# Optimization experiments

Measured on AMD Instinct MI355X. Metric: run time of the kernel, lower is better.

## Reference

```python
import jax, jax.numpy as jnp
import numpy as np

B, N, EN, EE = 2, 512, 128, 64
F = 64          # out_features * num_heads (shared by node and edge projections)
H = 8           # num_heads
D_NODE = 8.0    # out_node_features (softmax scale)
D_EDGE = 8.0    # out_edge_features (softmax scale)


def setup_inputs() -> dict:
    key = jax.random.key(0)
    ks = jax.random.split(key, 6)
    nodes = jax.random.normal(ks[0], (B, N, EN), dtype=jnp.float32)
    edges = jax.random.normal(ks[1], (B, N, N, EE), dtype=jnp.float32)
    node_mask = jnp.ones((B, N), dtype=bool)
    node_W = jax.random.normal(ks[2], (EN, F), dtype=jnp.float32) / np.sqrt(EN)
    node_b = jnp.zeros((F,), dtype=jnp.float32)
    edge_W = jax.random.normal(ks[3], (EE, F), dtype=jnp.float32) / np.sqrt(EE)
    edge_b = jnp.zeros((F,), dtype=jnp.float32)
    att_W = jax.random.normal(ks[4], (F, H), dtype=jnp.float32) / np.sqrt(F)
    return {"nodes": nodes, "edges": edges, "node_mask": node_mask,
            "node_W": node_W, "node_b": node_b,
            "edge_W": edge_W, "edge_b": edge_b, "att_W": att_W}


def reference(nodes, edges, node_mask, node_W, node_b, edge_W, edge_b, att_W):
    nf = nodes @ node_W + node_b                      # [b,n,F]
    ef = edges @ edge_W + edge_b                      # [b,n,n,F]
    q = nf @ att_W                                    # [b,n,H]
    eq = ef @ att_W                                   # [b,n,n,H]
    sn = jnp.einsum('bik,bjk->bij', q, q) / jnp.sqrt(jnp.float32(D_NODE))
    se = jnp.einsum('bik,bijk->bij', q, eq) / jnp.sqrt(jnp.float32(D_EDGE))
    m = node_mask[..., None].astype(sn.dtype)         # [b,n,1] (mask multiplies scores, as in source)
    wn = jax.nn.softmax(sn * m, axis=-1)              # [b,n,n]
    we = jax.nn.softmax(se * m, axis=-1)              # [b,n,n]
    awn = jnp.einsum('bij,bik->bjk', wn, nf)          # [b,n,F]
    aef = jnp.einsum('bij,bijk->bik', we, ef)         # [b,n,F]
    updated_nodes = nf + awn + aef
    awe = we[..., None] * ef                          # [b,n,n,F]
    anf = jnp.einsum('bij,bik->bijk', wn, nf)         # [b,n,n,F]
    updated_edges = ef + awe + anf
    out_nodes = jax.nn.elu(updated_nodes)
    out_edges = jax.nn.elu(updated_edges).reshape(edges.shape[0], edges.shape[1], edges.shape[2], -1)
    return out_nodes, out_edges
```

## Files before the change

kernel.cpp:

```cpp
#include <hip/hip_runtime.h>
#include <stdint.h>

#define BB 2
#define NN 512
#define ENF 128
#define EEF 64
#define FF 64
#define HH 8

#define WS_NF    0
#define WS_Q     65536
#define WS_V     73728
#define WS_EW    139264
#define WS_EB    143360
#define WS_M     143424
#define WS_STATS 143936
#define WS_FLAG  145984
#define WS_EWFH  145992
#define WS_EWFL  150088
#define WS_TOTAL 154184

__device__ __align__(16) float g_ws[WS_TOTAL];

using short8  = __attribute__((ext_vector_type(8))) short;
using floatx4 = __attribute__((ext_vector_type(4))) float;

__device__ __forceinline__ float bf2f(uint16_t u) {
  return __uint_as_float(((uint32_t)u) << 16);
}
__device__ __forceinline__ uint16_t f2bf(float f) {
  uint32_t u = __float_as_uint(f);
  return (uint16_t)((u + 0x7FFFu + ((u >> 16) & 1u)) >> 16);
}
__device__ __forceinline__ void split2(float f0, float f1, uint32_t& hi, uint32_t& lo) {
  uint16_t h0 = f2bf(f0), h1 = f2bf(f1);
  float r0 = f0 - bf2f(h0), r1 = f1 - bf2f(h1);
  uint16_t l0 = f2bf(r0), l1 = f2bf(r1);
  hi = (uint32_t)h0 | ((uint32_t)h1 << 16);
  lo = (uint32_t)l0 | ((uint32_t)l1 << 16);
}
__device__ __forceinline__ float load1(const void* p, size_t i, bool isf32) {
  return isf32 ? ((const float*)p)[i] : bf2f(((const uint16_t*)p)[i]);
}
__device__ __forceinline__ float elu(float x) {
  return x > 0.f ? x : expf(x) - 1.0f;
}

constexpr float INV_SQRT8 = 0.35355339059327373f;

__global__ __launch_bounds__(256) void k0_detect(
    const uint16_t* p0, int c0, const uint16_t* p1, int c1,
    const uint16_t* p2, int c2, const uint16_t* p3, int c3,
    const uint16_t* p4, int c4, const uint16_t* p5, int c5,
    const uint16_t* p6, int c6) {
  const uint16_t* ptrs[7] = {p0, p1, p2, p3, p4, p5, p6};
  const int cnts[7] = {c0, c1, c2, c3, c4, c5, c6};
  const int a = blockIdx.x;
  const uint16_t* e = ptrs[a];
  int S = cnts[a] / 2; if (S > 2048) S = 2048;
  const int t = threadIdx.x;
  int hi = 0, z0 = 0, nz1 = 0;
  for (int i = t; i < S; i += 256) {
    uint16_t h0 = e[2 * i], h1 = e[2 * i + 1];
    if (((h0 >> 7) & 0xFF) >= 0x90) hi++;
    if (h0 == 0) z0++;
    if (h1 != 0) nz1++;
  }
  for (int o = 32; o > 0; o >>= 1) {
    hi += __shfl_xor(hi, o); z0 += __shfl_xor(z0, o); nz1 += __shfl_xor(nz1, o);
  }
  __shared__ int r[3][4];
  if ((t & 63) == 0) { int w = t >> 6; r[0][w] = hi; r[1][w] = z0; r[2][w] = nz1; }
  __syncthreads();
  if (t == 0) {
    int H  = r[0][0] + r[0][1] + r[0][2] + r[0][3];
    int Z  = r[1][0] + r[1][1] + r[1][2] + r[1][3];
    int NZ = r[2][0] + r[2][1] + r[2][2] + r[2][3];
    g_ws[WS_FLAG + a] =
        (H > S / 16 || (Z * 8 > S * 3 && NZ * 8 > S * 3)) ? 1.0f : 0.0f;
  }
}

__global__ __launch_bounds__(256) void k1_nf_q_v(
    const void* __restrict__ nodes, const void* __restrict__ node_W,
    const void* __restrict__ node_b, const void* __restrict__ att_W,
    const void* __restrict__ edge_W, const void* __restrict__ edge_b) {
  float* nf  = g_ws + WS_NF;
  float* q   = g_ws + WS_Q;
  float* v   = g_ws + WS_V;
  float* eWf = g_ws + WS_EW;
  float* ebf = g_ws + WS_EB;
  float* Mf  = g_ws + WS_M;
  const float* fl = g_ws + WS_FLAG;
  const bool fNodes = fl[1] != 0.f, fNW = fl[2] != 0.f, fNB = fl[3] != 0.f;
  const bool fEW = fl[4] != 0.f, fEB = fl[5] != 0.f, fAW = fl[6] != 0.f;
  const int t    = threadIdx.x;
  const int lane = t & 63;
  const int wv   = t >> 6;
  const int bi   = blockIdx.x * 4 + wv;
  __shared__ float nd[4][ENF];
  __shared__ float nf_s[4][FF];
  __shared__ float q_s[4][HH];
  nd[wv][lane]      = load1(nodes, (size_t)bi * ENF + lane, fNodes);
  nd[wv][lane + 64] = load1(nodes, (size_t)bi * ENF + lane + 64, fNodes);
  __syncthreads();
  float acc = load1(node_b, lane, fNB);
#pragma unroll 8
  for (int e = 0; e < ENF; ++e) acc += nd[wv][e] * load1(node_W, e * FF + lane, fNW);
  nf[bi * FF + lane] = acc;
  nf_s[wv][lane] = acc;
  __syncthreads();
  if (lane < HH) {
    float s = 0.f;
#pragma unroll
    for (int k = 0; k < FF; ++k) s += nf_s[wv][k] * load1(att_W, k * HH + lane, fAW);
    q[bi * HH + lane] = s;
    q_s[wv][lane] = s;
  }
  __syncthreads();
  {
    float s = 0.f;
#pragma unroll
    for (int h = 0; h < HH; ++h) s += load1(att_W, lane * HH + h, fAW) * q_s[wv][h];
    v[bi * FF + lane] = s * INV_SQRT8;
  }
  if (blockIdx.x == 0) {
    if (wv == 0) {
      for (int idx = lane; idx < EEF * FF; idx += 64)
        eWf[idx] = load1(edge_W, idx, fEW);
      ebf[lane] = load1(edge_b, lane, fEB);
    } else if (wv == 1) {
      float mrow[HH];
#pragma unroll
      for (int h = 0; h < HH; ++h) mrow[h] = 0.f;
      for (int k = 0; k < FF; ++k) {
        float w = load1(edge_W, (size_t)lane * FF + k, fEW);
#pragma unroll
        for (int h = 0; h < HH; ++h) mrow[h] += w * load1(att_W, k * HH + h, fAW);
      }
#pragma unroll
      for (int h = 0; h < HH; ++h) Mf[lane * HH + h] = mrow[h];
    } else {
      const int ks = wv - 2;
      uint32_t* dH = (uint32_t*)(g_ws + WS_EWFH);
      uint32_t* dL = (uint32_t*)(g_ws + WS_EWFL);
#pragma unroll
      for (int nt = 0; nt < 4; ++nt) {
        const int f = ks * 4 + nt;
        const int n = nt * 16 + (lane & 15);
        const int e0 = ks * 32 + ((lane >> 4) << 3);
#pragma unroll
        for (int jj = 0; jj < 4; ++jj) {
          float w0 = load1(edge_W, (size_t)(e0 + 2 * jj) * FF + n, fEW);
          float w1 = load1(edge_W, (size_t)(e0 + 2 * jj + 1) * FF + n, fEW);
          uint32_t hi, lo;
          split2(w0, w1, hi, lo);
          dH[(f * 64 + lane) * 4 + jj] = hi;
          dL[(f * 64 + lane) * 4 + jj] = lo;
        }
      }
    }
  }
}

__global__ __launch_bounds__(256) void k2_stats() {
  const float* ws_q = g_ws + WS_Q;
  float* st = g_ws + WS_STATS;
  const int bi = blockIdx.x;
  const int b  = bi >> 9;
  const int t  = threadIdx.x;
  __shared__ float red[4];
  __shared__ float red2[4];
  const float* qi = ws_q + bi * HH;
  const float q0 = qi[0], q1 = qi[1], q2 = qi[2], q3 = qi[3];
  const float q4 = qi[4], q5 = qi[5], q6 = qi[6], q7 = qi[7];
  const float* qb = ws_q + ((size_t)(b << 9)) * HH;
  const int j0 = t, j1 = t + 256;
  const float* qa = qb + j0 * HH;
  float s0 = (q0*qa[0]+q1*qa[1]+q2*qa[2]+q3*qa[3]+q4*qa[4]+q5*qa[5]+q6*qa[6]+q7*qa[7]) * INV_SQRT8;
  const float* qc = qb + j1 * HH;
  float s1 = (q0*qc[0]+q1*qc[1]+q2*qc[2]+q3*qc[3]+q4*qc[4]+q5*qc[5]+q6*qc[6]+q7*qc[7]) * INV_SQRT8;
  float m = fmaxf(s0, s1);
  for (int o = 32; o > 0; o >>= 1) m = fmaxf(m, __shfl_xor(m, o));
  if ((t & 63) == 0) red[t >> 6] = m;
  __syncthreads();
  m = fmaxf(fmaxf(red[0], red[1]), fmaxf(red[2], red[3]));
  float p0 = expf(s0 - m), p1 = expf(s1 - m);
  float s = p0 + p1;
  for (int o = 32; o > 0; o >>= 1) s += __shfl_xor(s, o);
  if ((t & 63) == 0) red2[t >> 6] = s;
  __syncthreads();
  if (t == 0) {
    st[bi * 2]     = m;
    st[bi * 2 + 1] = 1.0f / (red2[0] + red2[1] + red2[2] + red2[3]);
  }
}

__global__ __launch_bounds__(1024, 1) void k4_main(
    const void* __restrict__ edges, float* __restrict__ out) {
  const bool isf32 = g_ws[WS_FLAG + 0] != 0.0f;
  const float* nf  = g_ws + WS_NF;
  const float* qws = g_ws + WS_Q;
  const float* ebf = g_ws + WS_EB;
  const float* Mf  = g_ws + WS_M;
  const float* st  = g_ws + WS_STATS;
  const int bi = blockIdx.x;
  const int t  = threadIdx.x;
  const int lane = t & 63;
  const int wv = t >> 6;

  __shared__ uint4 bH_s[8][64];
  __shared__ uint4 bL_s[8][64];
  __shared__ float wn_s[NN];
  __shared__ float wcol_s[NN];
  __shared__ float se_s[NN];
  __shared__ float u_s[EEF];
  __shared__ float nfi_s[FF];
  __shared__ float red[16], red2[16];
  __shared__ float aef_w[16][FF];
  __shared__ float awn_w[16][FF];

  if (t < 512) ((uint4*)bH_s)[t] = ((const uint4*)(g_ws + WS_EWFH))[t];
  else         ((uint4*)bL_s)[t - 512] = ((const uint4*)(g_ws + WS_EWFL))[t - 512];
  if (t < FF) nfi_s[t] = nf[bi * FF + t];
  if (t >= 128 && t < 128 + EEF) {
    const int c = t - 128;
    const float* qi2 = qws + bi * HH;
    const float* mr = Mf + c * HH;
    float s = 0.f;
#pragma unroll
    for (int h = 0; h < HH; ++h) s += mr[h] * qi2[h];
    u_s[c] = s * INV_SQRT8;
  }
  const float m_i   = st[bi * 2];
  const float inv_i = st[bi * 2 + 1];
  const float* qi = qws + bi * HH;
  const float q0 = qi[0], q1 = qi[1], q2 = qi[2], q3 = qi[3];
  const float q4 = qi[4], q5 = qi[5], q6 = qi[6], q7 = qi[7];
  const int bbase = (bi >> 9) << 9;
  if (t < NN) {
    const float* qt = qws + ((size_t)(bbase + t)) * HH;
    const float s_t = (q0*qt[0]+q1*qt[1]+q2*qt[2]+q3*qt[3]
                      +q4*qt[4]+q5*qt[5]+q6*qt[6]+q7*qt[7]) * INV_SQRT8;
    wn_s[t] = expf(s_t - m_i) * inv_i;
    const float2 stt = ((const float2*)st)[bbase + t];
    wcol_s[t] = expf(s_t - stt.x) * stt.y;
  }
  __syncthreads();

  float eb_n[4], nf_v[4];
#pragma unroll
  for (int nt = 0; nt < 4; ++nt) {
    eb_n[nt] = ebf[nt * 16 + (lane & 15)];
    nf_v[nt] = nfi_s[nt * 16 + (lane & 15)];
  }
  const int g8 = (lane >> 4) << 3;
  float ulo[8], uhi[8];
#pragma unroll
  for (int j = 0; j < 8; ++j) { ulo[j] = u_s[g8 + j]; uhi[j] = u_s[g8 + 32 + j]; }

  floatx4 acc[2][4];
  if (isf32) {
    const float* ef32 = (const float*)edges + ((size_t)bi * NN + wv * 32) * EEF;
#pragma unroll
    for (int mt = 0; mt < 2; ++mt) {
      const float* ap = ef32 + (size_t)(mt * 16 + (lane & 15)) * EEF + g8;
      const float4 x0 = *(const float4*)(ap);
      const float4 x1 = *(const float4*)(ap + 4);
      const float4 x2 = *(const float4*)(ap + 32);
      const float4 x3 = *(const float4*)(ap + 36);
      float p = x0.x*ulo[0] + x0.y*ulo[1] + x0.z*ulo[2] + x0.w*ulo[3]
              + x1.x*ulo[4] + x1.y*ulo[5] + x1.z*ulo[6] + x1.w*ulo[7]
              + x2.x*uhi[0] + x2.y*uhi[1] + x2.z*uhi[2] + x2.w*uhi[3]
              + x3.x*uhi[4] + x3.y*uhi[5] + x3.z*uhi[6] + x3.w*uhi[7];
      p += __shfl_xor(p, 16);
      p += __shfl_xor(p, 32);
      if (lane < 16) se_s[wv * 32 + mt * 16 + lane] = p;
      union { uint32_t u[4]; short8 s; } a0h, a0l, a1h, a1l;
      split2(x0.x, x0.y, a0h.u[0], a0l.u[0]);
      split2(x0.z, x0.w, a0h.u[1], a0l.u[1]);
      split2(x1.x, x1.y, a0h.u[2], a0l.u[2]);
      split2(x1.z, x1.w, a0h.u[3], a0l.u[3]);
      split2(x2.x, x2.y, a1h.u[0], a1l.u[0]);
      split2(x2.z, x2.w, a1h.u[1], a1l.u[1]);
      split2(x3.x, x3.y, a1h.u[2], a1l.u[2]);
      split2(x3.z, x3.w, a1h.u[3], a1l.u[3]);
#pragma unroll
      for (int nt = 0; nt < 4; ++nt) {
        const uint4 h0 = bH_s[nt][lane];
        const uint4 h1 = bH_s[4 + nt][lane];
        const uint4 l0 = bL_s[nt][lane];
        const uint4 l1 = bL_s[4 + nt][lane];
        floatx4 c = (floatx4){eb_n[nt], eb_n[nt], eb_n[nt], eb_n[nt]};
        c = __builtin_amdgcn_mfma_f32_16x16x32_bf16(a0h.s, *(const short8*)&h0, c, 0, 0, 0);
        c = __builtin_amdgcn_mfma_f32_16x16x32_bf16(a1h.s, *(const short8*)&h1, c, 0, 0, 0);
        c = __builtin_amdgcn_mfma_f32_16x16x32_bf16(a0h.s, *(const short8*)&l0, c, 0, 0, 0);
        c = __builtin_amdgcn_mfma_f32_16x16x32_bf16(a1h.s, *(const short8*)&l1, c, 0, 0, 0);
        c = __builtin_amdgcn_mfma_f32_16x16x32_bf16(a0l.s, *(const short8*)&h0, c, 0, 0, 0);
        c = __builtin_amdgcn_mfma_f32_16x16x32_bf16(a1l.s, *(const short8*)&h1, c, 0, 0, 0);
        acc[mt][nt] = c;
      }
    }
  } else {
    const uint16_t* eb16 = (const uint16_t*)edges + ((size_t)bi * NN + wv * 32) * EEF;
#pragma unroll
    for (int mt = 0; mt < 2; ++mt) {
      const uint16_t* ap = eb16 + (size_t)(mt * 16 + (lane & 15)) * EEF + g8;
      const short8 a0 = *(const short8*)(ap);
      const short8 a1 = *(const short8*)(ap + 32);
      float p = 0.f;
#pragma unroll
      for (int j = 0; j < 8; ++j) {
        p += bf2f((uint16_t)a0[j]) * ulo[j];
        p += bf2f((uint16_t)a1[j]) * uhi[j];
      }
      p += __shfl_xor(p, 16);
      p += __shfl_xor(p, 32);
      if (lane < 16) se_s[wv * 32 + mt * 16 + lane] = p;
#pragma unroll
      for (int nt = 0; nt < 4; ++nt) {
        const uint4 h0 = bH_s[nt][lane];
        const uint4 h1 = bH_s[4 + nt][lane];
        const uint4 l0 = bL_s[nt][lane];
        const uint4 l1 = bL_s[4 + nt][lane];
        floatx4 c = (floatx4){eb_n[nt], eb_n[nt], eb_n[nt], eb_n[nt]};
        c = __builtin_amdgcn_mfma_f32_16x16x32_bf16(a0, *(const short8*)&h0, c, 0, 0, 0);
        c = __builtin_amdgcn_mfma_f32_16x16x32_bf16(a1, *(const short8*)&h1, c, 0, 0, 0);
        c = __builtin_amdgcn_mfma_f32_16x16x32_bf16(a0, *(const short8*)&l0, c, 0, 0, 0);
        c = __builtin_amdgcn_mfma_f32_16x16x32_bf16(a1, *(const short8*)&l1, c, 0, 0, 0);
        acc[mt][nt] = c;
      }
    }
  }
  __syncthreads();

  const float sev = (t < NN) ? se_s[t] : -3.0e38f;
  float m = sev;
  for (int o = 32; o > 0; o >>= 1) m = fmaxf(m, __shfl_xor(m, o));
  if (lane == 0) red[wv] = m;
  __syncthreads();
  m = red[0];
#pragma unroll
  for (int w = 1; w < 16; ++w) m = fmaxf(m, red[w]);
  const float p = (t < NN) ? expf(sev - m) : 0.f;
  float ssum = p;
  for (int o = 32; o > 0; o >>= 1) ssum += __shfl_xor(ssum, o);
  if (lane == 0) red2[wv] = ssum;
  if (t < NN) se_s[t] = p;
  __syncthreads();
  float tot = red2[0];
#pragma unroll
  for (int w = 1; w < 16; ++w) tot += red2[w];
  const float inv_tot = 1.0f / tot;

  float aef_v[4] = {0.f, 0.f, 0.f, 0.f};
  float* oute = out + 65536 + ((size_t)bi * NN + wv * 32) * EEF;
#pragma unroll
  for (int mt = 0; mt < 2; ++mt) {
#pragma unroll
    for (int r = 0; r < 4; ++r) {
      const int row = mt * 16 + ((lane >> 4) << 2) + r;
      const float we = se_s[wv * 32 + row] * inv_tot;
      const float wnr = wn_s[wv * 32 + row];
      const float onewe = 1.0f + we;
#pragma unroll
      for (int nt = 0; nt < 4; ++nt) {
        const float c = acc[mt][nt][r];
        oute[(size_t)row * EEF + nt * 16 + (lane & 15)] = elu(c * onewe + wnr * nf_v[nt]);
        aef_v[nt] = fmaf(we, c, aef_v[nt]);
      }
    }
  }
#pragma unroll
  for (int nt = 0; nt < 4; ++nt) {
    float g = aef_v[nt];
    g += __shfl_xor(g, 16);
    g += __shfl_xor(g, 32);
    if (lane < 16) aef_w[wv][nt * 16 + lane] = g;
  }

  float awn_acc = 0.f;
  {
    const float* nfb = nf + (size_t)bbase * FF;
#pragma unroll 8
    for (int jj = 0; jj < 32; ++jj) {
      const int j = wv * 32 + jj;
      awn_acc = fmaf(wcol_s[j], nfb[(size_t)j * FF + lane], awn_acc);
    }
  }
  awn_w[wv][lane] = awn_acc;
  __syncthreads();

  if (t < FF) {
    float sum = nfi_s[t];
#pragma unroll
    for (int w = 0; w < 16; ++w) sum += aef_w[w][t] + awn_w[w][t];
    out[bi * FF + t] = elu(sum);
  }
}

extern "C" void kernel_launch(void* const* d_in, const int* in_sizes, int n_in,
                              void* d_out, int out_size, void* d_ws, size_t ws_size,
                              hipStream_t stream) {
  const void* nodes = nullptr; const void* edges = nullptr;
  const void* node_W = nullptr; const void* node_b = nullptr;
  const void* edge_W = nullptr; const void* edge_b = nullptr;
  const void* att_W = nullptr;
  int bias_seen = 0;
  for (int i = 0; i < n_in; ++i) {
    switch (in_sizes[i]) {
      case 33554432: edges  = d_in[i]; break;
      case 131072:   nodes  = d_in[i]; break;
      case 8192:     node_W = d_in[i]; break;
      case 4096:     edge_W = d_in[i]; break;
      case 512:      att_W  = d_in[i]; break;
      case 64:       if (bias_seen++ == 0) node_b = d_in[i]; else edge_b = d_in[i]; break;
      default: break;
    }
  }
  float* out = (float*)d_out;

  k0_detect<<<dim3(7), dim3(256), 0, stream>>>(
      (const uint16_t*)edges, 33554432, (const uint16_t*)nodes, 131072,
      (const uint16_t*)node_W, 8192, (const uint16_t*)node_b, 64,
      (const uint16_t*)edge_W, 4096, (const uint16_t*)edge_b, 64,
      (const uint16_t*)att_W, 512);
  k1_nf_q_v<<<dim3(BB * NN / 4), dim3(256), 0, stream>>>(nodes, node_W, node_b,
                                                         att_W, edge_W, edge_b);
  k2_stats<<<dim3(BB * NN), dim3(256), 0, stream>>>();
  k4_main<<<dim3(BB * NN), dim3(1024), 0, stream>>>(edges, out);
}
```

Before: 320.3 us.

## Prefetch edge tiles at kernel start, truncate split, drop unused v computation

The main kernel now issues its global loads of the edge tile into registers at the very start, before the shared-memory setup and softmax-weight computation. The aim is to overlap that memory latency with the setup work. The fp32 hi/lo bf16 split now truncates with bit masks instead of rounding, which costs fewer ALU ops but gives a slightly different split; the error stays in the lo residual. The unused v projection and its extra barrier are removed from k1.

```diff
diff --git a/kernel.cpp b/kernel.cpp
--- a/kernel.cpp
+++ b/kernel.cpp
@@ -38,6 +38,12 @@
   uint16_t l0 = f2bf(r0), l1 = f2bf(r1);
   hi = (uint32_t)h0 | ((uint32_t)h1 << 16);
   lo = (uint32_t)l0 | ((uint32_t)l1 << 16);
+}
+__device__ __forceinline__ void split2t(uint32_t u0, uint32_t u1, uint32_t& hi, uint32_t& lo) {
+  hi = (u0 >> 16) | (u1 & 0xFFFF0000u);
+  float r0 = __uint_as_float(u0) - __uint_as_float(u0 & 0xFFFF0000u);
+  float r1 = __uint_as_float(u1) - __uint_as_float(u1 & 0xFFFF0000u);
+  lo = (__float_as_uint(r0) >> 16) | (__float_as_uint(r1) & 0xFFFF0000u);
 }
 __device__ __forceinline__ float load1(const void* p, size_t i, bool isf32) {
   return isf32 ? ((const float*)p)[i] : bf2f(((const uint16_t*)p)[i]);
@@ -87,7 +93,6 @@
     const void* __restrict__ edge_W, const void* __restrict__ edge_b) {
   float* nf  = g_ws + WS_NF;
   float* q   = g_ws + WS_Q;
-  float* v   = g_ws + WS_V;
   float* eWf = g_ws + WS_EW;
   float* ebf = g_ws + WS_EB;
   float* Mf  = g_ws + WS_M;
@@ -100,7 +105,6 @@
   const int bi   = blockIdx.x * 4 + wv;
   __shared__ float nd[4][ENF];
   __shared__ float nf_s[4][FF];
-  __shared__ float q_s[4][HH];
   nd[wv][lane]      = load1(nodes, (size_t)bi * ENF + lane, fNodes);
   nd[wv][lane + 64] = load1(nodes, (size_t)bi * ENF + lane + 64, fNodes);
   __syncthreads();
@@ -115,14 +119,6 @@
 #pragma unroll
     for (int k = 0; k < FF; ++k) s += nf_s[wv][k] * load1(att_W, k * HH + lane, fAW);
     q[bi * HH + lane] = s;
-    q_s[wv][lane] = s;
-  }
-  __syncthreads();
-  {
-    float s = 0.f;
-#pragma unroll
-    for (int h = 0; h < HH; ++h) s += load1(att_W, lane * HH + h, fAW) * q_s[wv][h];
-    v[bi * FF + lane] = s * INV_SQRT8;
   }
   if (blockIdx.x == 0) {
     if (wv == 0) {
@@ -208,6 +204,29 @@
   const int t  = threadIdx.x;
   const int lane = t & 63;
   const int wv = t >> 6;
+  const int g8 = (lane >> 4) << 3;
+
+  uint4 raw[8];
+  if (isf32) {
+    const float* ef32 = (const float*)edges + ((size_t)bi * NN + wv * 32) * EEF;
+#pragma unroll
+    for (int mt = 0; mt < 2; ++mt) {
+      const float* ap = ef32 + (size_t)(mt * 16 + (lane & 15)) * EEF + g8;
+      raw[mt * 4 + 0] = *(const uint4*)(ap);
+      raw[mt * 4 + 1] = *(const uint4*)(ap + 4);
+      raw[mt * 4 + 2] = *(const uint4*)(ap + 32);
+      raw[mt * 4 + 3] = *(const uint4*)(ap + 36);
+    }
+  } else {
+    const uint16_t* eb16 = (const uint16_t*)edges + ((size_t)bi * NN + wv * 32) * EEF;
+#pragma unroll
+    for (int mt = 0; mt < 2; ++mt) {
+      const uint16_t* ap = eb16 + (size_t)(mt * 16 + (lane & 15)) * EEF + g8;
+      raw[mt * 4 + 0] = *(const uint4*)(ap);
+      raw[mt * 4 + 1] = *(const uint4*)(ap + 32);
+      raw[mt * 4 + 2] = raw[mt * 4 + 3] = (uint4){0, 0, 0, 0};
+    }
+  }
 
   __shared__ uint4 bH_s[8][64];
   __shared__ uint4 bL_s[8][64];
@@ -254,37 +273,36 @@
     eb_n[nt] = ebf[nt * 16 + (lane & 15)];
     nf_v[nt] = nfi_s[nt * 16 + (lane & 15)];
   }
-  const int g8 = (lane >> 4) << 3;
   float ulo[8], uhi[8];
 #pragma unroll
   for (int j = 0; j < 8; ++j) { ulo[j] = u_s[g8 + j]; uhi[j] = u_s[g8 + 32 + j]; }
 
   floatx4 acc[2][4];
   if (isf32) {
-    const float* ef32 = (const float*)edges + ((size_t)bi * NN + wv * 32) * EEF;
 #pragma unroll
     for (int mt = 0; mt < 2; ++mt) {
-      const float* ap = ef32 + (size_t)(mt * 16 + (lane & 15)) * EEF + g8;
-      const float4 x0 = *(const float4*)(ap);
-      const float4 x1 = *(const float4*)(ap + 4);
-      const float4 x2 = *(const float4*)(ap + 32);
-      const float4 x3 = *(const float4*)(ap + 36);
-      float p = x0.x*ulo[0] + x0.y*ulo[1] + x0.z*ulo[2] + x0.w*ulo[3]
-              + x1.x*ulo[4] + x1.y*ulo[5] + x1.z*ulo[6] + x1.w*ulo[7]
-              + x2.x*uhi[0] + x2.y*uhi[1] + x2.z*uhi[2] + x2.w*uhi[3]
-              + x3.x*uhi[4] + x3.y*uhi[5] + x3.z*uhi[6] + x3.w*uhi[7];
+      const uint4 x0 = raw[mt * 4 + 0], x1 = raw[mt * 4 + 1];
+      const uint4 x2 = raw[mt * 4 + 2], x3 = raw[mt * 4 + 3];
+      float p = __uint_as_float(x0.x)*ulo[0] + __uint_as_float(x0.y)*ulo[1]
+              + __uint_as_float(x0.z)*ulo[2] + __uint_as_float(x0.w)*ulo[3]
+              + __uint_as_float(x1.x)*ulo[4] + __uint_as_float(x1.y)*ulo[5]
+              + __uint_as_float(x1.z)*ulo[6] + __uint_as_float(x1.w)*ulo[7]
+              + __uint_as_float(x2.x)*uhi[0] + __uint_as_float(x2.y)*uhi[1]
+              + __uint_as_float(x2.z)*uhi[2] + __uint_as_float(x2.w)*uhi[3]
+              + __uint_as_float(x3.x)*uhi[4] + __uint_as_float(x3.y)*uhi[5]
+              + __uint_as_float(x3.z)*uhi[6] + __uint_as_float(x3.w)*uhi[7];
       p += __shfl_xor(p, 16);
       p += __shfl_xor(p, 32);
       if (lane < 16) se_s[wv * 32 + mt * 16 + lane] = p;
       union { uint32_t u[4]; short8 s; } a0h, a0l, a1h, a1l;
-      split2(x0.x, x0.y, a0h.u[0], a0l.u[0]);
-      split2(x0.z, x0.w, a0h.u[1], a0l.u[1]);
-      split2(x1.x, x1.y, a0h.u[2], a0l.u[2]);
-      split2(x1.z, x1.w, a0h.u[3], a0l.u[3]);
-      split2(x2.x, x2.y, a1h.u[0], a1l.u[0]);
-      split2(x2.z, x2.w, a1h.u[1], a1l.u[1]);
-      split2(x3.x, x3.y, a1h.u[2], a1l.u[2]);
-      split2(x3.z, x3.w, a1h.u[3], a1l.u[3]);
+      split2t(x0.x, x0.y, a0h.u[0], a0l.u[0]);
+      split2t(x0.z, x0.w, a0h.u[1], a0l.u[1]);
+      split2t(x1.x, x1.y, a0h.u[2], a0l.u[2]);
+      split2t(x1.z, x1.w, a0h.u[3], a0l.u[3]);
+      split2t(x2.x, x2.y, a1h.u[0], a1l.u[0]);
+      split2t(x2.z, x2.w, a1h.u[1], a1l.u[1]);
+      split2t(x3.x, x3.y, a1h.u[2], a1l.u[2]);
+      split2t(x3.z, x3.w, a1h.u[3], a1l.u[3]);
 #pragma unroll
       for (int nt = 0; nt < 4; ++nt) {
         const uint4 h0 = bH_s[nt][lane];
@@ -302,12 +320,11 @@
       }
     }
   } else {
-    const uint16_t* eb16 = (const uint16_t*)edges + ((size_t)bi * NN + wv * 32) * EEF;
 #pragma unroll
     for (int mt = 0; mt < 2; ++mt) {
-      const uint16_t* ap = eb16 + (size_t)(mt * 16 + (lane & 15)) * EEF + g8;
-      const short8 a0 = *(const short8*)(ap);
-      const short8 a1 = *(const short8*)(ap + 32);
+      const uint4 r0 = raw[mt * 4 + 0], r1 = raw[mt * 4 + 1];
+      const short8 a0 = *(const short8*)&r0;
+      const short8 a1 = *(const short8*)&r1;
       float p = 0.f;
 #pragma unroll
       for (int j = 0; j < 8; ++j) {
```

Measured after the change: 326.5 us. About the same (+1.9%).
